# Optimization experiments

Hardware: AMD Instinct MI355X
Metric: run time of the kernel (lower is better)

Reference implementation:

```python
import jax, jax.numpy as jnp
import numpy as np
from jax import lax

B, N, S, K = 8, 4096, 1024, 32   # batch, points, npoint (FPS samples), nsample (ball query)
RADIUS = 0.15
ALPHA = 0.2                      # LeakyReLU negative slope
EPS = 1e-5                       # BatchNorm eps
MLP = [64, 64, 128]
D_IN = 6                         # per-point feature dim


def _index_points(p, idx):
    # p: [B, N, C]; idx: [B, ...] -> [B, ..., C]
    return jax.vmap(lambda pp, ii: pp[ii])(p, idx)


def _fps(xyz, npoint):
    # Farthest point sampling. Deterministic start at index 0 (original uses randint).
    b, n, _ = xyz.shape
    def step(carry, _):
        dist, far = carry
        c = xyz[jnp.arange(b), far]                    # [b,3] current centroid
        d = jnp.sum((xyz - c[:, None, :]) ** 2, -1)    # [b,n]
        dist = jnp.minimum(dist, d)
        return (dist, jnp.argmax(dist, -1).astype(jnp.int32)), far
    init = (jnp.full((b, n), 1e10, xyz.dtype), jnp.zeros((b,), jnp.int32))
    _, cent = lax.scan(step, init, None, length=npoint)
    return cent.T                                       # [b, npoint]


def _ball_query(radius, nsample, xyz, new_xyz):
    n = xyz.shape[1]
    # squared distances [B,S,N]
    sqr = (jnp.sum(new_xyz ** 2, -1)[:, :, None]
           + jnp.sum(xyz ** 2, -1)[:, None, :]
           - 2.0 * jnp.einsum('bsc,bnc->bsn', new_xyz, xyz))
    idx = jnp.where(sqr > radius * radius, n,
                    jnp.arange(n, dtype=jnp.int32)[None, None, :])
    idx = jnp.sort(idx, axis=-1)[:, :, :nsample]        # [B,S,K]
    return jnp.where(idx == n, idx[:, :, :1], idx)      # pad misses with first hit


def _mlp_bn_relu(x, w, b, g, be, m, v):
    # 1x1 Conv2d == linear on last axis; BatchNorm in eval mode with running stats.
    x = jnp.einsum('...c,oc->...o', x, w) + b
    x = g * (x - m) * lax.rsqrt(v + EPS) + be
    return jax.nn.relu(x)


def reference(xyz, points, w0, b0, g0, be0, m0, v0, w1, b1, g1, be1, m1, v1,
              w2, b2, g2, be2, m2, v2, a):
    params = [(w0, b0, g0, be0, m0, v0), (w1, b1, g1, be1, m1, v1),
              (w2, b2, g2, be2, m2, v2)]
    xyz_t = xyz.transpose(0, 2, 1)                      # [B,N,3]
    pts = points.transpose(0, 2, 1)                     # [B,N,D]

    fps_idx = _fps(xyz_t, S)                            # [B,S]
    new_xyz = _index_points(xyz_t, fps_idx)             # [B,S,3]
    idx = _ball_query(RADIUS, K, xyz_t, new_xyz)        # [B,S,K]
    grouped_xyz = _index_points(xyz_t, idx)             # [B,S,K,3]
    grouped_pts = _index_points(pts, idx)               # [B,S,K,D]
    fps_pts = _index_points(pts, fps_idx)               # [B,S,D]

    center = jnp.concatenate([new_xyz, fps_pts], -1)                       # [B,S,3+D]
    neigh = jnp.concatenate([grouped_xyz - new_xyz[:, :, None, :],
                             grouped_pts], -1)                             # [B,S,K,3+D]

    for (w, b, g, be, m, v) in params:
        center = _mlp_bn_relu(center, w, b, g, be, m, v)
        neigh = _mlp_bn_relu(neigh, w, b, g, be, m, v)

    # Graph attention: LeakyReLU scores, softmax over neighbors, weighted sum.
    dp = new_xyz[:, :, None, :] - grouped_xyz                              # [B,S,K,3]
    dh = center[:, :, None, :] - neigh                                     # [B,S,K,Dout]
    e = jax.nn.leaky_relu(jnp.concatenate([dp, dh], -1) @ a, ALPHA)        # [B,S,K,Dout]
    att = jax.nn.softmax(e, axis=2)                                        # over K
    out = jnp.sum(att * neigh, axis=2)                                     # [B,S,Dout]

    return new_xyz.transpose(0, 2, 1), out.transpose(0, 2, 1)              # [B,3,S],[B,Dout,S]


def setup_inputs() -> dict:
    key = jax.random.key(0)
    ks = jax.random.split(key, 32)
    inp = {
        'xyz': jax.random.uniform(ks[0], (B, 3, N), jnp.float32),
        'points': jax.random.normal(ks[1], (B, D_IN, N), jnp.float32),
    }
    last = 3 + D_IN
    j = 2
    for i, out_c in enumerate(MLP):
        scale = np.sqrt(2.0 / (last + out_c)).astype(np.float32)
        inp[f'w{i}'] = jax.random.normal(ks[j], (out_c, last), jnp.float32) * scale; j += 1
        inp[f'b{i}'] = jax.random.normal(ks[j], (out_c,), jnp.float32) * 0.01; j += 1
        inp[f'g{i}'] = 1.0 + 0.1 * jax.random.normal(ks[j], (out_c,), jnp.float32); j += 1
        inp[f'be{i}'] = 0.1 * jax.random.normal(ks[j], (out_c,), jnp.float32); j += 1
        inp[f'm{i}'] = 0.1 * jax.random.normal(ks[j], (out_c,), jnp.float32); j += 1
        inp[f'v{i}'] = 0.5 + jax.random.uniform(ks[j], (out_c,), jnp.float32); j += 1
        last = out_c
    inp['a'] = jax.random.normal(ks[j], (3 + MLP[-1], MLP[-1]), jnp.float32) * np.sqrt(2.0 / (3 + 2 * MLP[-1])).astype(np.float32)
    return inp


if __name__ == '__main__':
    o = reference(**setup_inputs())
    print(o[0].shape, o[1].shape)
```

## Files before the change

kernel.cpp:

```cpp
#include <hip/hip_runtime.h>

#define NB  8
#define NPT 4096
#define NS  1024
#define NK  32
#define DIN 6
#define QPB 32
#define MEGA_THREADS 512

#define OFF_A   0
#define OFF_W1  16768
#define OFF_W2  20864
#define OFF_W0  29056
#define OFF_H1  29632
#define OFF_H2  31808
#define OFF_U   33984
#define FLT_TOT 38208
#define SMEM_BYTES (FLT_TOT * 4)

__device__ __forceinline__ float bnrelu(float acc, const float* __restrict__ bb,
                                        const float* __restrict__ gg,
                                        const float* __restrict__ be,
                                        const float* __restrict__ mm,
                                        const float* __restrict__ vv, int oc) {
  float t = (acc + bb[oc]) - mm[oc];
  float val = gg[oc] * t * rsqrtf(vv[oc] + 1e-5f) + be[oc];
  return fmaxf(val, 0.0f);
}

__device__ __forceinline__ float wave64_max(float x) {
  const int NEG1 = 0xbf800000;
  int v;
  v = __builtin_amdgcn_update_dpp(NEG1, __float_as_int(x), 0x111, 0xf, 0xf, false);
  x = fmaxf(x, __int_as_float(v));
  v = __builtin_amdgcn_update_dpp(NEG1, __float_as_int(x), 0x112, 0xf, 0xf, false);
  x = fmaxf(x, __int_as_float(v));
  v = __builtin_amdgcn_update_dpp(NEG1, __float_as_int(x), 0x114, 0xf, 0xf, false);
  x = fmaxf(x, __int_as_float(v));
  v = __builtin_amdgcn_update_dpp(NEG1, __float_as_int(x), 0x118, 0xf, 0xf, false);
  x = fmaxf(x, __int_as_float(v));
  v = __builtin_amdgcn_update_dpp(NEG1, __float_as_int(x), 0x142, 0xa, 0xf, false);
  x = fmaxf(x, __int_as_float(v));
  v = __builtin_amdgcn_update_dpp(NEG1, __float_as_int(x), 0x143, 0xc, 0xf, false);
  x = fmaxf(x, __int_as_float(v));
  return __int_as_float(__builtin_amdgcn_readlane(__float_as_int(x), 63));
}

__global__ __launch_bounds__(512) void fps_kernel(const float* __restrict__ xyz,
                                                  int* __restrict__ fps_idx,
                                                  float* __restrict__ nxyz,
                                                  float* __restrict__ out0) {
  const int b = blockIdx.x;
  const int t = threadIdx.x;
  const int lane = t & 63, wid = t >> 6;
  const float* xb = xyz + (size_t)b * 3 * NPT;

  __shared__ float s_x[NPT], s_y[NPT], s_z[NPT];
  __shared__ __align__(16) float s_red[2][8][2];
  __shared__ float s_ox[NS], s_oy[NS], s_oz[NS];
  __shared__ int s_fi[NS];

  float px[8], py[8], pz[8], dist[8];
  const int base = t * 8;
#pragma unroll
  for (int j = 0; j < 8; ++j) {
    px[j] = xb[base + j];
    py[j] = xb[NPT + base + j];
    pz[j] = xb[2 * NPT + base + j];
    dist[j] = 1e10f;
  }
  for (int i = t; i < NPT; i += 512) {
    s_x[i] = xb[i];
    s_y[i] = xb[NPT + i];
    s_z[i] = xb[2 * NPT + i];
  }
  __syncthreads();

  int far = 0;
  float cx = xb[0], cy = xb[NPT], cz = xb[2 * NPT];

  for (int s = 0; s < NS; ++s) {
    if (t == 0) {
      s_ox[s] = cx; s_oy[s] = cy; s_oz[s] = cz; s_fi[s] = far;
    }
    float bv = -1.0f;
    int bi = 0;
#pragma unroll
    for (int j = 0; j < 8; ++j) {
      float dx = __fsub_rn(px[j], cx);
      float dy = __fsub_rn(py[j], cy);
      float dz = __fsub_rn(pz[j], cz);
      float d = __fadd_rn(__fadd_rn(__fmul_rn(dx, dx), __fmul_rn(dy, dy)),
                          __fmul_rn(dz, dz));
      float nd = fminf(dist[j], d);
      dist[j] = nd;
      bi = (nd > bv) ? (base + j) : bi;
      bv = fmaxf(bv, nd);
    }
    float mv = wave64_max(bv);
    unsigned long long mmask = __ballot(bv == mv);
    int src = __ffsll(mmask) - 1;
    int wi = __shfl(bi, src);

    const int p = s & 1;
    if (lane == 0) {
      s_red[p][wid][0] = mv;
      s_red[p][wid][1] = __int_as_float(wi);
    }
    __syncthreads();

    float4 q0 = *(const float4*)&s_red[p][0][0];
    float4 q1 = *(const float4*)&s_red[p][2][0];
    float4 q2 = *(const float4*)&s_red[p][4][0];
    float4 q3 = *(const float4*)&s_red[p][6][0];
    float va, vb, vc, vd; int ia, ib, ic, id;
    { bool g = q0.z > q0.x; va = g ? q0.z : q0.x;
      ia = g ? __float_as_int(q0.w) : __float_as_int(q0.y); }
    { bool g = q1.z > q1.x; vb = g ? q1.z : q1.x;
      ib = g ? __float_as_int(q1.w) : __float_as_int(q1.y); }
    { bool g = q2.z > q2.x; vc = g ? q2.z : q2.x;
      ic = g ? __float_as_int(q2.w) : __float_as_int(q2.y); }
    { bool g = q3.z > q3.x; vd = g ? q3.z : q3.x;
      id = g ? __float_as_int(q3.w) : __float_as_int(q3.y); }
    { bool g = vb > va; va = g ? vb : va; ia = g ? ib : ia; }
    { bool g = vd > vc; vc = g ? vd : vc; ic = g ? id : ic; }
    { bool g = vc > va; va = g ? vc : va; ia = g ? ic : ia; }
    far = ia;
    cx = s_x[far]; cy = s_y[far]; cz = s_z[far];
  }

  __syncthreads();
  for (int i = t; i < NS; i += 512) {
    float X = s_ox[i], Y = s_oy[i], Z = s_oz[i];
    out0[((size_t)b * 3 + 0) * NS + i] = X;
    out0[((size_t)b * 3 + 1) * NS + i] = Y;
    out0[((size_t)b * 3 + 2) * NS + i] = Z;
    nxyz[((size_t)b * NS + i) * 3 + 0] = X;
    nxyz[((size_t)b * NS + i) * 3 + 1] = Y;
    nxyz[((size_t)b * NS + i) * 3 + 2] = Z;
    fps_idx[b * NS + i] = s_fi[i];
  }
}

__global__ __launch_bounds__(64) void center_kernel(
    const float* __restrict__ points, const float* __restrict__ nxyz,
    const int* __restrict__ fps_idx,
    const float* __restrict__ w0, const float* __restrict__ b0,
    const float* __restrict__ g0, const float* __restrict__ be0,
    const float* __restrict__ m0, const float* __restrict__ v0,
    const float* __restrict__ w1, const float* __restrict__ b1,
    const float* __restrict__ g1, const float* __restrict__ be1,
    const float* __restrict__ m1, const float* __restrict__ v1,
    const float* __restrict__ w2, const float* __restrict__ b2,
    const float* __restrict__ g2, const float* __restrict__ be2,
    const float* __restrict__ m2, const float* __restrict__ v2,
    const float* __restrict__ a, float* __restrict__ ceA) {
  const int bs = blockIdx.x;
  const int b = bs >> 10;
  const int t = threadIdx.x;

  __shared__ float ci[9];
  __shared__ float ch1[64];
  __shared__ float ch2[64];
  __shared__ float ch3[128];

  if (t < 9) {
    ci[t] = (t < 3) ? nxyz[(size_t)bs * 3 + t]
                    : points[((size_t)b * DIN + (t - 3)) * NPT + fps_idx[bs]];
  }
  __syncthreads();
  {
    float acc = 0.f;
#pragma unroll
    for (int c = 0; c < 9; ++c) acc = fmaf(ci[c], w0[t * 9 + c], acc);
    ch1[t] = bnrelu(acc, b0, g0, be0, m0, v0, t);
  }
  __syncthreads();
  {
    float acc = 0.f;
#pragma unroll 8
    for (int c = 0; c < 64; ++c) acc = fmaf(ch1[c], w1[t * 64 + c], acc);
    ch2[t] = bnrelu(acc, b1, g1, be1, m1, v1, t);
  }
  __syncthreads();
  for (int oc = t; oc < 128; oc += 64) {
    float acc = 0.f;
#pragma unroll 8
    for (int c = 0; c < 64; ++c) acc = fmaf(ch2[c], w2[oc * 64 + c], acc);
    ch3[oc] = bnrelu(acc, b2, g2, be2, m2, v2, oc);
  }
  __syncthreads();
  for (int oc = t; oc < 128; oc += 64) {
    float acc = 0.f;
#pragma unroll 8
    for (int c = 0; c < 128; ++c) acc = fmaf(ch3[c], a[(3 + c) * 128 + oc], acc);
    ceA[(size_t)bs * 128 + oc] = acc;
  }
}

__global__ __launch_bounds__(256) void ballq_kernel(
    const float* __restrict__ xyz, const float* __restrict__ nxyz,
    float4* __restrict__ gq) {
  const int bs = blockIdx.x;
  const int b = bs >> 10;
  const int t = threadIdx.x;
  const int lane = t & 63;
  const int wid = t >> 6;

  __shared__ int s_widx[4][NK];
  __shared__ int s_wc[4];

  const float* xb = xyz + (size_t)b * 3 * NPT;
  const float cx = nxyz[(size_t)bs * 3 + 0];
  const float cy = nxyz[(size_t)bs * 3 + 1];
  const float cz = nxyz[(size_t)bs * 3 + 2];

  {
    const float R2 = (float)(0.15 * 0.15);
    float s2c = __fadd_rn(__fadd_rn(__fmul_rn(cx, cx), __fmul_rn(cy, cy)),
                          __fmul_rn(cz, cz));
    int wcnt = 0;
    for (int g = 0; g < 16; ++g) {
      int n = wid * 1024 + g * 64 + lane;
      float x = xb[n];
      float y = xb[NPT + n];
      float z = xb[2 * NPT + n];
      float pn2 = __fadd_rn(__fadd_rn(__fmul_rn(x, x), __fmul_rn(y, y)),
                            __fmul_rn(z, z));
      float dot = fmaf(cz, z, fmaf(cy, y, __fmul_rn(cx, x)));
      float sqr = __fsub_rn(__fadd_rn(s2c, pn2), __fmul_rn(2.0f, dot));
      bool hit = !(sqr > R2);
      unsigned long long mm = __ballot(hit);
      int pos = wcnt + __popcll(mm & ((1ull << lane) - 1ull));
      if (hit && pos < NK) s_widx[wid][pos] = n;
      wcnt += __popcll(mm);
      if (wcnt >= NK) break;
    }
    if (lane == 0) s_wc[wid] = (wcnt < NK) ? wcnt : NK;
  }
  __syncthreads();

  if (t < NK) {
    int c0 = s_wc[0], c1 = s_wc[1], c2 = s_wc[2], c3 = s_wc[3];
    int total = c0 + c1 + c2 + c3;
    int cc[4] = {c0, c1, c2, c3};
    int p = (t < total) ? t : 0;
    int w = 0;
    while (w < 3 && p >= cc[w]) { p -= cc[w]; ++w; }
    int n = s_widx[w][p];
    float gx = __fsub_rn(xb[n], cx);
    float gy = __fsub_rn(xb[NPT + n], cy);
    float gz = __fsub_rn(xb[2 * NPT + n], cz);
    gq[(size_t)bs * NK + t] = make_float4(gx, gy, gz, __int_as_float(n));
  }
}

__global__ __launch_bounds__(MEGA_THREADS) void mega_kernel(
    const float* __restrict__ points, const float* __restrict__ ceA,
    const float4* __restrict__ gq,
    const float* __restrict__ w0, const float* __restrict__ b0,
    const float* __restrict__ g0, const float* __restrict__ be0,
    const float* __restrict__ m0, const float* __restrict__ v0,
    const float* __restrict__ w1, const float* __restrict__ b1,
    const float* __restrict__ g1, const float* __restrict__ be1,
    const float* __restrict__ m1, const float* __restrict__ v1,
    const float* __restrict__ w2, const float* __restrict__ b2,
    const float* __restrict__ g2, const float* __restrict__ be2,
    const float* __restrict__ m2, const float* __restrict__ v2,
    const float* __restrict__ a, float* __restrict__ out1) {
  extern __shared__ float lds[];
  float* s_a  = lds + OFF_A;
  float* s_w1 = lds + OFF_W1;
  float* s_w2 = lds + OFF_W2;
  float* s_w0 = lds + OFF_W0;
  float* s_h1 = lds + OFF_H1;
  float* s_h2 = lds + OFF_H2;
  float* s_u  = lds + OFF_U;

  const int t = threadIdx.x;
  const int k = t & 31;
  const int g16 = t >> 5;

  {
    const float4* srcA = (const float4*)a;
    float4* dstA = (float4*)s_a;
    for (int i = t; i < 4192; i += MEGA_THREADS) dstA[i] = srcA[i];
    const float4* src1 = (const float4*)w1;
    float4* dst1 = (float4*)s_w1;
    for (int i = t; i < 1024; i += MEGA_THREADS) dst1[i] = src1[i];
    const float4* src2 = (const float4*)w2;
    float4* dst2 = (float4*)s_w2;
    for (int i = t; i < 2048; i += MEGA_THREADS) dst2[i] = src2[i];
    for (int i = t; i < 576; i += MEGA_THREADS) s_w0[i] = w0[i];
  }
  __syncthreads();

  for (int q = 0; q < QPB; ++q) {
    const int bs = blockIdx.x * QPB + q;
    const int b = bs >> 10;
    const int s = bs & 1023;

    float4 gv = gq[(size_t)bs * NK + k];
    const int n = __float_as_int(gv.w);

    {
      float in0[9];
      in0[0] = gv.x; in0[1] = gv.y; in0[2] = gv.z;
      const float* pb = points + (size_t)b * DIN * NPT + n;
#pragma unroll
      for (int c = 0; c < 6; ++c) in0[3 + c] = pb[(size_t)c * NPT];
      int oc0 = g16 * 4;
      float acc[4];
#pragma unroll
      for (int j = 0; j < 4; ++j) {
        float a0 = 0.f;
#pragma unroll
        for (int c = 0; c < 9; ++c)
          a0 = fmaf(in0[c], s_w0[(oc0 + j) * 9 + c], a0);
        acc[j] = bnrelu(a0, b0, g0, be0, m0, v0, oc0 + j);
      }
      *(float4*)&s_h1[k * 68 + oc0] = make_float4(acc[0], acc[1], acc[2], acc[3]);
    }
    __syncthreads();

    {
      int oc0 = g16 * 4;
      float acc[4] = {0.f, 0.f, 0.f, 0.f};
      const float4* row = (const float4*)&s_h1[k * 68];
#pragma unroll 4
      for (int c4 = 0; c4 < 16; ++c4) {
        float4 hv = row[c4];
#pragma unroll
        for (int j = 0; j < 4; ++j) {
          float4 wv = *(const float4*)&s_w1[(oc0 + j) * 64 + c4 * 4];
          acc[j] = fmaf(hv.x, wv.x, acc[j]);
          acc[j] = fmaf(hv.y, wv.y, acc[j]);
          acc[j] = fmaf(hv.z, wv.z, acc[j]);
          acc[j] = fmaf(hv.w, wv.w, acc[j]);
        }
      }
#pragma unroll
      for (int j = 0; j < 4; ++j)
        acc[j] = bnrelu(acc[j], b1, g1, be1, m1, v1, oc0 + j);
      *(float4*)&s_h2[k * 68 + oc0] = make_float4(acc[0], acc[1], acc[2], acc[3]);
    }
    __syncthreads();

    {
      int oc0 = g16 * 8;
      float acc[8] = {0.f, 0.f, 0.f, 0.f, 0.f, 0.f, 0.f, 0.f};
      const float4* row = (const float4*)&s_h2[k * 68];
#pragma unroll 2
      for (int c4 = 0; c4 < 16; ++c4) {
        float4 hv = row[c4];
#pragma unroll
        for (int j = 0; j < 8; ++j) {
          float4 wv = *(const float4*)&s_w2[(oc0 + j) * 64 + c4 * 4];
          acc[j] = fmaf(hv.x, wv.x, acc[j]);
          acc[j] = fmaf(hv.y, wv.y, acc[j]);
          acc[j] = fmaf(hv.z, wv.z, acc[j]);
          acc[j] = fmaf(hv.w, wv.w, acc[j]);
        }
      }
#pragma unroll
      for (int j = 0; j < 8; ++j)
        acc[j] = bnrelu(acc[j], b2, g2, be2, m2, v2, oc0 + j);
      float4* orow = (float4*)&s_u[k * 132 + oc0];
      orow[0] = make_float4(acc[0], acc[1], acc[2], acc[3]);
      orow[1] = make_float4(acc[4], acc[5], acc[6], acc[7]);
      if (t < NK) {
        s_u[t * 132 + 128] = gv.x;
        s_u[t * 132 + 129] = gv.y;
        s_u[t * 132 + 130] = gv.z;
        s_u[t * 132 + 131] = 0.f;
      }
    }
    __syncthreads();

    {
      int oc0 = g16 * 8;
      float acc[8] = {0.f, 0.f, 0.f, 0.f, 0.f, 0.f, 0.f, 0.f};
      const float4* urow = (const float4*)&s_u[k * 132];
      for (int r4 = 0; r4 < 33; ++r4) {
        float4 uv = urow[r4];
        int r = r4 * 4;
#pragma unroll
        for (int cc = 0; cc < 4; ++cc) {
          int rr = r + cc;
          int arow = (rr < 128) ? (rr + 3) : (rr - 128);
          float uc = (cc == 0) ? uv.x : (cc == 1) ? uv.y : (cc == 2) ? uv.z : uv.w;
          const float4* ap = (const float4*)&s_a[arow * 128 + oc0];
          float4 av0 = ap[0], av1 = ap[1];
          acc[0] = fmaf(uc, av0.x, acc[0]);
          acc[1] = fmaf(uc, av0.y, acc[1]);
          acc[2] = fmaf(uc, av0.z, acc[2]);
          acc[3] = fmaf(uc, av0.w, acc[3]);
          acc[4] = fmaf(uc, av1.x, acc[4]);
          acc[5] = fmaf(uc, av1.y, acc[5]);
          acc[6] = fmaf(uc, av1.z, acc[6]);
          acc[7] = fmaf(uc, av1.w, acc[7]);
        }
      }

      float ce[8], h3[8];
      {
        float4 cv0 = *(const float4*)&ceA[(size_t)bs * 128 + oc0];
        float4 cv1 = *(const float4*)&ceA[(size_t)bs * 128 + oc0 + 4];
        ce[0] = cv0.x; ce[1] = cv0.y; ce[2] = cv0.z; ce[3] = cv0.w;
        ce[4] = cv1.x; ce[5] = cv1.y; ce[6] = cv1.z; ce[7] = cv1.w;
        float4 hv0 = *(const float4*)&s_u[k * 132 + oc0];
        float4 hv1 = *(const float4*)&s_u[k * 132 + oc0 + 4];
        h3[0] = hv0.x; h3[1] = hv0.y; h3[2] = hv0.z; h3[3] = hv0.w;
        h3[4] = hv1.x; h3[5] = hv1.y; h3[6] = hv1.z; h3[7] = hv1.w;
      }

      float* outb = out1 + (size_t)b * 128 * NS + s;
#pragma unroll
      for (int j = 0; j < 8; ++j) {
        float e = ce[j] - acc[j];
        e = (e >= 0.f) ? e : 0.2f * e;
        float mx = e;
#pragma unroll
        for (int off = 16; off > 0; off >>= 1)
          mx = fmaxf(mx, __shfl_xor(mx, off));
        float p = expf(e - mx);
        float num = p * h3[j];
        float den = p;
#pragma unroll
        for (int off = 16; off > 0; off >>= 1) {
          num += __shfl_xor(num, off);
          den += __shfl_xor(den, off);
        }
        if (k == 0) outb[(size_t)(oc0 + j) * NS] = num / den;
      }
    }
  }
}

extern "C" void kernel_launch(void* const* d_in, const int* in_sizes, int n_in,
                              void* d_out, int out_size, void* d_ws,
                              size_t ws_size, hipStream_t stream) {
  (void)in_sizes; (void)n_in; (void)out_size; (void)ws_size;
  const float* xyz = (const float*)d_in[0];
  const float* points = (const float*)d_in[1];
  const float* w0 = (const float*)d_in[2];
  const float* b0 = (const float*)d_in[3];
  const float* g0 = (const float*)d_in[4];
  const float* be0 = (const float*)d_in[5];
  const float* m0 = (const float*)d_in[6];
  const float* v0 = (const float*)d_in[7];
  const float* w1 = (const float*)d_in[8];
  const float* b1 = (const float*)d_in[9];
  const float* g1 = (const float*)d_in[10];
  const float* be1 = (const float*)d_in[11];
  const float* m1 = (const float*)d_in[12];
  const float* v1 = (const float*)d_in[13];
  const float* w2 = (const float*)d_in[14];
  const float* b2 = (const float*)d_in[15];
  const float* g2 = (const float*)d_in[16];
  const float* be2 = (const float*)d_in[17];
  const float* m2 = (const float*)d_in[18];
  const float* v2 = (const float*)d_in[19];
  const float* a = (const float*)d_in[20];

  float* out0 = (float*)d_out;
  float* out1 = out0 + (size_t)NB * 3 * NS;

  int* fps = (int*)d_ws;
  float* nxyz = (float*)((char*)d_ws + 32768);
  float* ceA = (float*)((char*)d_ws + 131072);
  float4* gq = (float4*)((char*)d_ws + 131072 + 4194304);

  hipFuncSetAttribute(reinterpret_cast<const void*>(mega_kernel),
                      hipFuncAttributeMaxDynamicSharedMemorySize, SMEM_BYTES);

  fps_kernel<<<NB, 512, 0, stream>>>(xyz, fps, nxyz, out0);
  ballq_kernel<<<NB * NS, 256, 0, stream>>>(xyz, nxyz, gq);
  center_kernel<<<NB * NS, 64, 0, stream>>>(points, nxyz, fps,
      w0, b0, g0, be0, m0, v0, w1, b1, g1, be1, m1, v1,
      w2, b2, g2, be2, m2, v2, a, ceA);
  mega_kernel<<<NB * NS / QPB, MEGA_THREADS, SMEM_BYTES, stream>>>(
      points, ceA, gq,
      w0, b0, g0, be0, m0, v0, w1, b1, g1, be1, m1, v1,
      w2, b2, g2, be2, m2, v2, a, out1);
}
```

Baseline: 1.265 ms.

## Register-block two neighbors per thread and prefetch next query's gather

Remaps the MLP layers 2-3 and the attention matvec so each thread handles two neighbor rows (kk and kk+16) for half as many output channels. Each LDS weight load is then reused across two rows, and the softmax shuffle reductions shrink from 5 to 4 steps. It also prefetches the next query's grouped coordinates and point features into registers during the current iteration, hiding global gather latency. The cost is more live registers and a different LDS access pattern, which may bring bank conflicts on the s_h1/s_h2 row reads.

Result: faster. 1.132 ms (-10.5%).

```diff
diff --git a/kernel.cpp b/kernel.cpp
--- a/kernel.cpp
+++ b/kernel.cpp
@@ -280,6 +280,8 @@
   const int t = threadIdx.x;
   const int k = t & 31;
   const int g16 = t >> 5;
+  const int kk = t & 15;
+  const int gg = t >> 4;
 
   {
     const float4* srcA = (const float4*)a;
@@ -295,20 +297,31 @@
   }
   __syncthreads();
 
+  const int bs0 = blockIdx.x * QPB;
+
+  float4 gv = gq[(size_t)bs0 * NK + k];
+  float pts[6];
+  {
+    int n = __float_as_int(gv.w);
+    const float* pb = points + (size_t)(bs0 >> 10) * DIN * NPT + n;
+#pragma unroll
+    for (int c = 0; c < 6; ++c) pts[c] = pb[(size_t)c * NPT];
+  }
+
   for (int q = 0; q < QPB; ++q) {
-    const int bs = blockIdx.x * QPB + q;
+    const int bs = bs0 + q;
     const int b = bs >> 10;
     const int s = bs & 1023;
 
-    float4 gv = gq[(size_t)bs * NK + k];
-    const int n = __float_as_int(gv.w);
+    const int qn = (q + 1 < QPB) ? (q + 1) : q;
+    const int bsn = bs0 + qn;
+    float4 gv_next = gq[(size_t)bsn * NK + k];
 
     {
       float in0[9];
       in0[0] = gv.x; in0[1] = gv.y; in0[2] = gv.z;
-      const float* pb = points + (size_t)b * DIN * NPT + n;
-#pragma unroll
-      for (int c = 0; c < 6; ++c) in0[3 + c] = pb[(size_t)c * NPT];
+#pragma unroll
+      for (int c = 0; c < 6; ++c) in0[3 + c] = pts[c];
       int oc0 = g16 * 4;
       float acc[4];
 #pragma unroll
@@ -323,51 +336,78 @@
     }
     __syncthreads();
 
+    float pts_next[6];
     {
-      int oc0 = g16 * 4;
-      float acc[4] = {0.f, 0.f, 0.f, 0.f};
-      const float4* row = (const float4*)&s_h1[k * 68];
+      int nn = __float_as_int(gv_next.w);
+      const float* pbn = points + (size_t)(bsn >> 10) * DIN * NPT + nn;
+#pragma unroll
+      for (int c = 0; c < 6; ++c) pts_next[c] = pbn[(size_t)c * NPT];
+    }
+
+    {
+      int oc0 = gg * 2;
+      float a0[2] = {0.f, 0.f}, a1[2] = {0.f, 0.f};
+      const float4* row0 = (const float4*)&s_h1[kk * 68];
+      const float4* row1 = (const float4*)&s_h1[(kk + 16) * 68];
 #pragma unroll 4
       for (int c4 = 0; c4 < 16; ++c4) {
-        float4 hv = row[c4];
+        float4 h0 = row0[c4];
+        float4 h1 = row1[c4];
+#pragma unroll
+        for (int j = 0; j < 2; ++j) {
+          float4 wv = *(const float4*)&s_w1[(oc0 + j) * 64 + c4 * 4];
+          a0[j] = fmaf(h0.x, wv.x, a0[j]);
+          a0[j] = fmaf(h0.y, wv.y, a0[j]);
+          a0[j] = fmaf(h0.z, wv.z, a0[j]);
+          a0[j] = fmaf(h0.w, wv.w, a0[j]);
+          a1[j] = fmaf(h1.x, wv.x, a1[j]);
+          a1[j] = fmaf(h1.y, wv.y, a1[j]);
+          a1[j] = fmaf(h1.z, wv.z, a1[j]);
+          a1[j] = fmaf(h1.w, wv.w, a1[j]);
+        }
+      }
+#pragma unroll
+      for (int j = 0; j < 2; ++j) {
+        a0[j] = bnrelu(a0[j], b1, g1, be1, m1, v1, oc0 + j);
+        a1[j] = bnrelu(a1[j], b1, g1, be1, m1, v1, oc0 + j);
+      }
+      s_h2[kk * 68 + oc0] = a0[0];
+      s_h2[kk * 68 + oc0 + 1] = a0[1];
+      s_h2[(kk + 16) * 68 + oc0] = a1[0];
+      s_h2[(kk + 16) * 68 + oc0 + 1] = a1[1];
+    }
+    __syncthreads();
+
+    {
+      int oc0 = gg * 4;
+      float a0[4] = {0.f, 0.f, 0.f, 0.f}, a1[4] = {0.f, 0.f, 0.f, 0.f};
+      const float4* row0 = (const float4*)&s_h2[kk * 68];
+      const float4* row1 = (const float4*)&s_h2[(kk + 16) * 68];
+#pragma unroll 4
+      for (int c4 = 0; c4 < 16; ++c4) {
+        float4 h0 = row0[c4];
+        float4 h1 = row1[c4];
 #pragma unroll
         for (int j = 0; j < 4; ++j) {
-          float4 wv = *(const float4*)&s_w1[(oc0 + j) * 64 + c4 * 4];
-          acc[j] = fmaf(hv.x, wv.x, acc[j]);
-          acc[j] = fmaf(hv.y, wv.y, acc[j]);
-          acc[j] = fmaf(hv.z, wv.z, acc[j]);
-          acc[j] = fmaf(hv.w, wv.w, acc[j]);
+          float4 wv = *(const float4*)&s_w2[(oc0 + j) * 64 + c4 * 4];
+          a0[j] = fmaf(h0.x, wv.x, a0[j]);
+          a0[j] = fmaf(h0.y, wv.y, a0[j]);
+          a0[j] = fmaf(h0.z, wv.z, a0[j]);
+          a0[j] = fmaf(h0.w, wv.w, a0[j]);
+          a1[j] = fmaf(h1.x, wv.x, a1[j]);
+          a1[j] = fmaf(h1.y, wv.y, a1[j]);
+          a1[j] = fmaf(h1.z, wv.z, a1[j]);
+          a1[j] = fmaf(h1.w, wv.w, a1[j]);
         }
       }
 #pragma unroll
-      for (int j = 0; j < 4; ++j)
-        acc[j] = bnrelu(acc[j], b1, g1, be1, m1, v1, oc0 + j);
-      *(float4*)&s_h2[k * 68 + oc0] = make_float4(acc[0], acc[1], acc[2], acc[3]);
-    }
-    __syncthreads();
-
-    {
-      int oc0 = g16 * 8;
-      float acc[8] = {0.f, 0.f, 0.f, 0.f, 0.f, 0.f, 0.f, 0.f};
-      const float4* row = (const float4*)&s_h2[k * 68];
-#pragma unroll 2
-      for (int c4 = 0; c4 < 16; ++c4) {
-        float4 hv = row[c4];
-#pragma unroll
-        for (int j = 0; j < 8; ++j) {
-          float4 wv = *(const float4*)&s_w2[(oc0 + j) * 64 + c4 * 4];
-          acc[j] = fmaf(hv.x, wv.x, acc[j]);
-          acc[j] = fmaf(hv.y, wv.y, acc[j]);
-          acc[j] = fmaf(hv.z, wv.z, acc[j]);
-          acc[j] = fmaf(hv.w, wv.w, acc[j]);
-        }
-      }
-#pragma unroll
-      for (int j = 0; j < 8; ++j)
-        acc[j] = bnrelu(acc[j], b2, g2, be2, m2, v2, oc0 + j);
-      float4* orow = (float4*)&s_u[k * 132 + oc0];
-      orow[0] = make_float4(acc[0], acc[1], acc[2], acc[3]);
-      orow[1] = make_float4(acc[4], acc[5], acc[6], acc[7]);
+      for (int j = 0; j < 4; ++j) {
+        a0[j] = bnrelu(a0[j], b2, g2, be2, m2, v2, oc0 + j);
+        a1[j] = bnrelu(a1[j], b2, g2, be2, m2, v2, oc0 + j);
+      }
+      *(float4*)&s_u[kk * 132 + oc0] = make_float4(a0[0], a0[1], a0[2], a0[3]);
+      *(float4*)&s_u[(kk + 16) * 132 + oc0] =
+          make_float4(a1[0], a1[1], a1[2], a1[3]);
       if (t < NK) {
         s_u[t * 132 + 128] = gv.x;
         s_u[t * 132 + 129] = gv.y;
@@ -378,62 +418,66 @@
     __syncthreads();
 
     {
-      int oc0 = g16 * 8;
-      float acc[8] = {0.f, 0.f, 0.f, 0.f, 0.f, 0.f, 0.f, 0.f};
-      const float4* urow = (const float4*)&s_u[k * 132];
+      int oc0 = gg * 4;
+      float a0[4] = {0.f, 0.f, 0.f, 0.f}, a1[4] = {0.f, 0.f, 0.f, 0.f};
+      const float4* urow0 = (const float4*)&s_u[kk * 132];
+      const float4* urow1 = (const float4*)&s_u[(kk + 16) * 132];
       for (int r4 = 0; r4 < 33; ++r4) {
-        float4 uv = urow[r4];
+        float4 uv0 = urow0[r4];
+        float4 uv1 = urow1[r4];
         int r = r4 * 4;
 #pragma unroll
         for (int cc = 0; cc < 4; ++cc) {
           int rr = r + cc;
           int arow = (rr < 128) ? (rr + 3) : (rr - 128);
-          float uc = (cc == 0) ? uv.x : (cc == 1) ? uv.y : (cc == 2) ? uv.z : uv.w;
-          const float4* ap = (const float4*)&s_a[arow * 128 + oc0];
-          float4 av0 = ap[0], av1 = ap[1];
-          acc[0] = fmaf(uc, av0.x, acc[0]);
-          acc[1] = fmaf(uc, av0.y, acc[1]);
-          acc[2] = fmaf(uc, av0.z, acc[2]);
-          acc[3] = fmaf(uc, av0.w, acc[3]);
-          acc[4] = fmaf(uc, av1.x, acc[4]);
-          acc[5] = fmaf(uc, av1.y, acc[5]);
-          acc[6] = fmaf(uc, av1.z, acc[6]);
-          acc[7] = fmaf(uc, av1.w, acc[7]);
+          float uc0 = (cc == 0) ? uv0.x : (cc == 1) ? uv0.y : (cc == 2) ? uv0.z : uv0.w;
+          float uc1 = (cc == 0) ? uv1.x : (cc == 1) ? uv1.y : (cc == 2) ? uv1.z : uv1.w;
+          float4 av = *(const float4*)&s_a[arow * 128 + oc0];
+          a0[0] = fmaf(uc0, av.x, a0[0]);
+          a0[1] = fmaf(uc0, av.y, a0[1]);
+          a0[2] = fmaf(uc0, av.z, a0[2]);
+          a0[3] = fmaf(uc0, av.w, a0[3]);
+          a1[0] = fmaf(uc1, av.x, a1[0]);
+          a1[1] = fmaf(uc1, av.y, a1[1]);
+          a1[2] = fmaf(uc1, av.z, a1[2]);
+          a1[3] = fmaf(uc1, av.w, a1[3]);
         }
       }
 
-      float ce[8], h3[8];
-      {
-        float4 cv0 = *(const float4*)&ceA[(size_t)bs * 128 + oc0];
-        float4 cv1 = *(const float4*)&ceA[(size_t)bs * 128 + oc0 + 4];
-        ce[0] = cv0.x; ce[1] = cv0.y; ce[2] = cv0.z; ce[3] = cv0.w;
-        ce[4] = cv1.x; ce[5] = cv1.y; ce[6] = cv1.z; ce[7] = cv1.w;
-        float4 hv0 = *(const float4*)&s_u[k * 132 + oc0];
-        float4 hv1 = *(const float4*)&s_u[k * 132 + oc0 + 4];
-        h3[0] = hv0.x; h3[1] = hv0.y; h3[2] = hv0.z; h3[3] = hv0.w;
-        h3[4] = hv1.x; h3[5] = hv1.y; h3[6] = hv1.z; h3[7] = hv1.w;
-      }
+      float4 cv = *(const float4*)&ceA[(size_t)bs * 128 + oc0];
+      float4 h0v = *(const float4*)&s_u[kk * 132 + oc0];
+      float4 h1v = *(const float4*)&s_u[(kk + 16) * 132 + oc0];
+      float ce[4] = {cv.x, cv.y, cv.z, cv.w};
+      float h0[4] = {h0v.x, h0v.y, h0v.z, h0v.w};
+      float h1[4] = {h1v.x, h1v.y, h1v.z, h1v.w};
 
       float* outb = out1 + (size_t)b * 128 * NS + s;
 #pragma unroll
-      for (int j = 0; j < 8; ++j) {
-        float e = ce[j] - acc[j];
-        e = (e >= 0.f) ? e : 0.2f * e;
-        float mx = e;
-#pragma unroll
-        for (int off = 16; off > 0; off >>= 1)
+      for (int j = 0; j < 4; ++j) {
+        float e0 = ce[j] - a0[j];
+        float e1 = ce[j] - a1[j];
+        e0 = (e0 >= 0.f) ? e0 : 0.2f * e0;
+        e1 = (e1 >= 0.f) ? e1 : 0.2f * e1;
+        float mx = fmaxf(e0, e1);
+#pragma unroll
+        for (int off = 8; off > 0; off >>= 1)
           mx = fmaxf(mx, __shfl_xor(mx, off));
-        float p = expf(e - mx);
-        float num = p * h3[j];
-        float den = p;
-#pragma unroll
-        for (int off = 16; off > 0; off >>= 1) {
+        float p0 = expf(e0 - mx);
+        float p1 = expf(e1 - mx);
+        float num = p0 * h0[j] + p1 * h1[j];
+        float den = p0 + p1;
+#pragma unroll
+        for (int off = 8; off > 0; off >>= 1) {
           num += __shfl_xor(num, off);
           den += __shfl_xor(den, off);
         }
-        if (k == 0) outb[(size_t)(oc0 + j) * NS] = num / den;
-      }
-    }
+        if (kk == 0) outb[(size_t)(oc0 + j) * NS] = num / den;
+      }
+    }
+
+    gv = gv_next;
+#pragma unroll
+    for (int c = 0; c < 6; ++c) pts[c] = pts_next[c];
   }
 }
 
```
